# Kernel optimization log

Hardware: AMD Instinct MI355X
Metric: run time of the kernel (lower is better)

## Reference

```python
import jax, jax.numpy as jnp
import numpy as np

D_MODEL = 1024
NUM_HEADS = 16
HEAD_DIM = D_MODEL // NUM_HEADS
BATCH = 2
SEQ = 2048


def setup_inputs() -> dict:
    key = jax.random.key(0)
    ks = jax.random.split(key, 9)
    s = 1.0 / np.sqrt(D_MODEL)
    X = jax.random.normal(ks[0], (BATCH, SEQ, D_MODEL), dtype=jnp.float32)
    # causal mask, broadcastable over batch and heads; masked_fill where mask == 0
    mask = jnp.tril(jnp.ones((SEQ, SEQ), dtype=jnp.int32))[None, None, :, :]
    Wq = jax.random.uniform(ks[1], (D_MODEL, D_MODEL), jnp.float32, -s, s)
    bq = jax.random.uniform(ks[2], (D_MODEL,), jnp.float32, -s, s)
    Wk = jax.random.uniform(ks[3], (D_MODEL, D_MODEL), jnp.float32, -s, s)
    bk = jax.random.uniform(ks[4], (D_MODEL,), jnp.float32, -s, s)
    Wv = jax.random.uniform(ks[5], (D_MODEL, D_MODEL), jnp.float32, -s, s)
    bv = jax.random.uniform(ks[6], (D_MODEL,), jnp.float32, -s, s)
    Wo = jax.random.uniform(ks[7], (D_MODEL, D_MODEL), jnp.float32, -s, s)
    bo = jax.random.uniform(ks[8], (D_MODEL,), jnp.float32, -s, s)
    return {"X": X, "mask": mask, "Wq": Wq, "bq": bq, "Wk": Wk, "bk": bk,
            "Wv": Wv, "bv": bv, "Wo": Wo, "bo": bo}


def reference(X, mask, Wq, bq, Wk, bk, Wv, bv, Wo, bo):
    B, S, _ = X.shape
    scale = 1.0 / np.sqrt(HEAD_DIM).astype(np.float32)

    def split_heads(t):  # [B,S,D] -> [B,H,S,Dh]
        return t.reshape(B, S, NUM_HEADS, HEAD_DIM).transpose(0, 2, 1, 3)

    q = split_heads(X @ Wq.T + bq)
    k = split_heads(X @ Wk.T + bk)
    v = split_heads(X @ Wv.T + bv)
    # [B,H,S,S] attention logits (explicitly materialized, as in the source)
    logits = jnp.einsum("bhqd,bhkd->bhqk", q, k) * scale
    logits = jnp.where(mask == 0, -jnp.inf, logits)
    attn = jax.nn.softmax(logits, axis=-1)  # dropout in eval mode: identity
    ctx = jnp.einsum("bhqk,bhkd->bhqd", attn, v)
    ctx = ctx.transpose(0, 2, 1, 3).reshape(B, S, D_MODEL)
    return ctx @ Wo.T + bo
```

## Files before the change

### kernel.cpp

```cpp
#include <hip/hip_runtime.h>


#define B_   2
#define S_   2048
#define H_   16
#define DH_  64
#define D_   1024
#define M_   (B_ * S_)

typedef __attribute__((ext_vector_type(8))) short short8;
typedef __attribute__((ext_vector_type(4))) short short4_t;
typedef float v4f __attribute__((ext_vector_type(4)));

__device__ __forceinline__ short f2bf(float f) {
    union { float f; unsigned u; } v; v.f = f;
    unsigned r = v.u + 0x7fffu + ((v.u >> 16) & 1u);
    return (short)(r >> 16);
}

#if __has_builtin(__builtin_amdgcn_exp2f)
#define EXP2(x) __builtin_amdgcn_exp2f(x)
#else
#define EXP2(x) exp2f(x)
#endif

__device__ __forceinline__ unsigned pack2(float a, float b) {
    return (__float_as_uint(a) >> 16) | (__float_as_uint(b) & 0xFFFF0000u);
}

__device__ __forceinline__ void gl2lds16(const short* g, short* l) {
    __builtin_amdgcn_global_load_lds(
        (const __attribute__((address_space(1))) unsigned int*)g,
        (__attribute__((address_space(3))) unsigned int*)l,
        16, 0, 0);
}

__global__ __launch_bounds__(256) void cast_kernel(
    const float* __restrict__ X,
    const float* __restrict__ Wq, const float* __restrict__ Wk,
    const float* __restrict__ Wv, const float* __restrict__ Wo,
    short* __restrict__ Xb, short* __restrict__ Wb)
{
    const int NX8 = (M_ * D_) / 8;
    const int NW8 = (D_ * D_) / 8;
    int idx = blockIdx.x * 256 + threadIdx.x;

    const float* src; short* dst; int off;
    if (idx < NX8) { src = X; dst = Xb; off = idx; }
    else {
        int r = idx - NX8;
        int sel = r >> 17;
        int o = r & (NW8 - 1);
        src = (sel == 0) ? Wq : (sel == 1) ? Wk : (sel == 2) ? Wv : Wo;
        dst = Wb + sel * (D_ * D_);
        off = o;
    }
    float4 f0 = ((const float4*)src)[off * 2];
    float4 f1 = ((const float4*)src)[off * 2 + 1];
    short8 s;
    s[0] = f2bf(f0.x); s[1] = f2bf(f0.y); s[2] = f2bf(f0.z); s[3] = f2bf(f0.w);
    s[4] = f2bf(f1.x); s[5] = f2bf(f1.y); s[6] = f2bf(f1.z); s[7] = f2bf(f1.w);
    *(short8*)(dst + (size_t)off * 8) = s;
}

template<int BN, int MODE>
__global__ __launch_bounds__(256) void gemm_kernel(
    const short* __restrict__ A, const short* __restrict__ W,
    const float* __restrict__ bq, const float* __restrict__ bk,
    const float* __restrict__ bv, void* __restrict__ out,
    int M, int N, int K)
{
    constexpr int SM = (MODE == 0) ? 18432 : (8192 + BN * 64);
    __shared__ __align__(16) short smem[SM];
    short* As = smem;
    short* Bs = smem + 8192;

    const int t    = threadIdx.x;
    const int lane = t & 63;
    const int wave = t >> 6;

    const int bid = blockIdx.x;
    const int by  = ((bid & 7) << 2) + ((bid >> 3) & 3);
    const int bx  = bid >> 5;
    const int m0 = by * 128;
    const int n0 = bx * BN;

    const int wm = (wave >> 1) * 64;
    const int wn = (wave & 1) * (BN / 2);
    constexpr int NJ  = BN / 32;
    constexpr int BIT = BN / 32;

    v4f acc[4][NJ] = {};

    const int rsub = lane >> 3;
    const int csw  = ((lane & 7) ^ rsub) * 8;
    const short* Ag = A + (size_t)(m0 + wave * 32 + rsub) * K + csw;
    const short* Wg = W + (size_t)(n0 + wave * (BN / 4) + rsub) * K + csw;
    short* Asw = As + (wave * 32) * 64;
    short* Bsw = Bs + (wave * (BN / 4)) * 64;

    const int lm = lane & 15;
    const int lg = lane >> 4;
    const int lm7 = lm & 7;

    for (int k0 = 0; k0 < K; k0 += 64) {
        #pragma unroll
        for (int i2 = 0; i2 < 4; ++i2)
            gl2lds16(Ag + (size_t)(i2 * 8) * K + k0, Asw + i2 * 512);
        #pragma unroll
        for (int i2 = 0; i2 < BIT; ++i2)
            gl2lds16(Wg + (size_t)(i2 * 8) * K + k0, Bsw + i2 * 512);
        __syncthreads();

        #pragma unroll
        for (int kk = 0; kk < 2; ++kk) {
            const int ch = (kk * 4 + lg) ^ lm7;
            short8 af[4], bf[NJ];
            #pragma unroll
            for (int i = 0; i < 4; ++i)
                af[i] = *(const short8*)((const char*)As + (wm + i * 16 + lm) * 128 + ch * 16);
            #pragma unroll
            for (int j = 0; j < NJ; ++j)
                bf[j] = *(const short8*)((const char*)Bs + (wn + j * 16 + lm) * 128 + ch * 16);
            #pragma unroll
            for (int i = 0; i < 4; ++i)
                #pragma unroll
                for (int j = 0; j < NJ; ++j)
                    acc[i][j] = __builtin_amdgcn_mfma_f32_16x16x32_bf16(af[i], bf[j], acc[i][j], 0, 0, 0);
        }
        __syncthreads();
    }

    const int sel = n0 >> 10;
    const float* bias = (MODE == 2) ? bq : (sel == 0) ? bq : (sel == 1) ? bk : bv;

    if constexpr (MODE == 2) {
        const int colb = n0 + wn + lm;
        const int rowb = m0 + wm + lg * 4;
        #pragma unroll
        for (int j = 0; j < NJ; ++j) {
            int col = colb + j * 16;
            float bv_ = bias[col];
            #pragma unroll
            for (int i = 0; i < 4; ++i)
                #pragma unroll
                for (int r = 0; r < 4; ++r)
                    ((float*)out)[(size_t)(rowb + i * 16 + r) * 1024 + col] = acc[i][j][r] + bv_;
        }
    } else {
        short* Es = smem + wave * (64 * 72);
        const int cb = (n0 + wn) & 1023;
        #pragma unroll
        for (int j = 0; j < 4; ++j) {
            float bv_ = bias[cb + j * 16 + lm];
            #pragma unroll
            for (int i = 0; i < 4; ++i)
                #pragma unroll
                for (int r = 0; r < 4; ++r) {
                    float vv = acc[i][j][r] + bv_;
                    if (sel == 0) vv *= 0.1803368867f;
                    if (sel < 2)
                        Es[(i * 16 + lg * 4 + r) * 72 + j * 16 + lm] = f2bf(vv);
                    else
                        Es[(j * 16 + lm) * 72 + i * 16 + lg * 4 + r] = f2bf(vv);
                }
        }
        __asm__ __volatile__("s_waitcnt lgkmcnt(0)" ::: "memory");
        short* outQKV = (short*)out;
        const int rl = lane >> 3;
        const int c8 = (lane & 7) * 8;
        const int h  = cb >> 6;
        const int b  = (m0 + wm) >> 11;
        const int bh = (b << 4) + h;
        if (sel < 2) {
            #pragma unroll
            for (int it = 0; it < 8; ++it) {
                int row_l = it * 8 + rl;
                short8 vrow = *(const short8*)&Es[row_l * 72 + c8];
                int s = (m0 + wm + row_l) & 2047;
                *(short8*)(outQKV + (size_t)sel * 4194304 +
                           ((size_t)bh * S_ + s) * DH_ + c8) = vrow;
            }
        } else {
            const int s0 = (m0 + wm) & 2047;
            #pragma unroll
            for (int it = 0; it < 8; ++it) {
                int d_l = it * 8 + rl;
                short8 vrow = *(const short8*)&Es[d_l * 72 + c8];
                *(short8*)(outQKV + (size_t)2 * 4194304 +
                           ((size_t)bh << 17) + ((size_t)d_l << 11) + s0 + c8) = vrow;
            }
        }
    }
}

__global__ __launch_bounds__(512, 2) void attn_kernel(
    const short* __restrict__ Q, const short* __restrict__ Kh,
    const short* __restrict__ Vt, short* __restrict__ ctx)
{
    __shared__ __align__(16) short sm[32768];

    const int t    = threadIdx.x;
    const int lane = t & 63;
    const int w    = t >> 6;
    const int wg   = w & 3;
    const int g    = w >> 2;
    const int bid  = blockIdx.x;

    const int lo  = bid & 255;
    const int xcd = lo & 7;
    const int idx = lo >> 3;
    const int bh  = (xcd << 2) + (idx & 3);
    const int jb  = idx >> 2;
    const int j   = (bid < 256) ? jb : (15 - jb);
    const int q0  = j * 128;
    const int nt  = j + 1;
    const int ha  = nt >> 1;
    const int mx  = nt - ha;
    const int pb  = g ? ha : 0;
    const int np  = g ? (nt - ha) : ha;
    const int qr0 = q0 + wg * 32;

    const int lm = lane & 15;
    const int lg = lane >> 4;

    short* Kt = sm + g * 16384;
    short* Vp = Kt + 8192;

    const short* Qb = Q  + (size_t)bh * S_ * DH_;
    const short* Kb = Kh + (size_t)bh * S_ * DH_;
    const short* Vb = Vt + ((size_t)bh << 17);

    const int rsubK = lane >> 3;
    const int cswK  = ((lane & 7) ^ rsubK) * 8;
    const int dV    = wg * 16 + (lane >> 2);
    const int s3V   = dV & 7;

    short8 qf[2][2];
    #pragma unroll
    for (int t2 = 0; t2 < 2; ++t2)
        #pragma unroll
        for (int kk = 0; kk < 2; ++kk)
            qf[t2][kk] = *(const short8*)(Qb + (size_t)(qr0 + t2 * 16 + lm) * DH_ + kk * 32 + lg * 8);

    float m_i[2] = {-1e30f, -1e30f}, l_i[2] = {0.f, 0.f};
    v4f o[2][4] = {};

    for (int tI = 0; tI < mx; ++tI) {
        const bool act   = tI < np;
        const int  kv0   = (pb + tI) * 128;
        const bool dpair = (g == 1) && (tI == mx - 1);

        if (act) {
            #pragma unroll
            for (int i2 = 0; i2 < 4; ++i2) {
                const int rb = wg * 32 + i2 * 8;
                gl2lds16(Kb + (size_t)(kv0 + rb + rsubK) * 64 + cswK, Kt + rb * 64);
            }
            short8 vld[4];
            #pragma unroll
            for (int m = 0; m < 4; ++m) {
                const int cm = (lane & 3) + 4 * m;
                vld[m] = *(const short8*)(Vb + (size_t)dV * 2048 + kv0 + cm * 8);
            }
            char* vrow = (char*)Vp + dV * 256;
            #pragma unroll
            for (int m = 0; m < 4; ++m) {
                const int cm = (lane & 3) + 4 * m;
                const int u  = cm >> 3, kk = (cm >> 2) & 1;
                const int q0off = ((cm & 1) << 4) + ((cm >> 1) & 1) * 4;
                const int bA = (u * 64 + kk * 32 + q0off) * 2;
                const int pA = ((((bA >> 4) ^ s3V) << 4) | (bA & 15));
                const int bB = bA + 16;
                const int pB = ((((bB >> 4) ^ s3V) << 4) | (bB & 15));
                *(short4_t*)(vrow + pA) = __builtin_shufflevector(vld[m], vld[m], 0, 1, 2, 3);
                *(short4_t*)(vrow + pB) = __builtin_shufflevector(vld[m], vld[m], 4, 5, 6, 7);
            }
        }
        __syncthreads();

        if (act) {
            short8 vf[2][2][4];
            #pragma unroll
            for (int u = 0; u < 2; ++u)
                #pragma unroll
                for (int kk = 0; kk < 2; ++kk)
                    #pragma unroll
                    for (int i = 0; i < 4; ++i) {
                        const int d = i * 16 + lm;
                        const int ch = (u * 8 + kk * 4 + lg) ^ (lm & 7);
                        vf[u][kk][i] = *(const short8*)((const char*)Vp + d * 256 + ch * 16);
                    }

            v4f sc[2][2][4] = {};
            #pragma unroll
            for (int u = 0; u < 2; ++u) {
                short8 kf[2][4];
                #pragma unroll
                for (int kk = 0; kk < 2; ++kk)
                    #pragma unroll
                    for (int jj = 0; jj < 4; ++jj) {
                        const int row = u * 64 + jj * 16 + lm;
                        const int ch  = (kk * 4 + lg) ^ (lm & 7);
                        kf[kk][jj] = *(const short8*)((const char*)Kt + row * 128 + ch * 16);
                    }
                #pragma unroll
                for (int kk = 0; kk < 2; ++kk)
                    #pragma unroll
                    for (int t2 = 0; t2 < 2; ++t2)
                        #pragma unroll
                        for (int jj = 0; jj < 4; ++jj)
                            sc[t2][u][jj] = __builtin_amdgcn_mfma_f32_16x16x32_bf16(kf[kk][jj], qf[t2][kk], sc[t2][u][jj], 0, 0, 0);
            }

            float alpha[2];
            short8 pf[2][2][2];
            #pragma unroll
            for (int t2 = 0; t2 < 2; ++t2) {
                float x[2][4][4];
                const int q = qr0 + t2 * 16 + lm;
                #pragma unroll
                for (int u = 0; u < 2; ++u)
                    #pragma unroll
                    for (int jj = 0; jj < 4; ++jj)
                        #pragma unroll
                        for (int r = 0; r < 4; ++r) {
                            float v = sc[t2][u][jj][r];
                            if (dpair && (kv0 + u * 64 + jj * 16 + lg * 4 + r > q)) v = -1e30f;
                            x[u][jj][r] = v;
                        }
                float m8[8];
                #pragma unroll
                for (int z = 0; z < 8; ++z) {
                    const float* xz = x[z >> 2][z & 3];
                    m8[z] = fmaxf(fmaxf(xz[0], xz[1]), fmaxf(xz[2], xz[3]));
                }
                float rm = fmaxf(fmaxf(fmaxf(m8[0], m8[1]), fmaxf(m8[2], m8[3])),
                                 fmaxf(fmaxf(m8[4], m8[5]), fmaxf(m8[6], m8[7])));
                rm = fmaxf(rm, __shfl_xor(rm, 16, 64));
                rm = fmaxf(rm, __shfl_xor(rm, 32, 64));

                const float mn = fmaxf(m_i[t2], rm);
                alpha[t2] = EXP2(m_i[t2] - mn);
                m_i[t2] = mn;

                float s8[8];
                #pragma unroll
                for (int z = 0; z < 8; ++z) {
                    float* xz = x[z >> 2][z & 3];
                    xz[0] = EXP2(xz[0] - mn); xz[1] = EXP2(xz[1] - mn);
                    xz[2] = EXP2(xz[2] - mn); xz[3] = EXP2(xz[3] - mn);
                    s8[z] = (xz[0] + xz[1]) + (xz[2] + xz[3]);
                }
                float rs = ((s8[0] + s8[1]) + (s8[2] + s8[3])) + ((s8[4] + s8[5]) + (s8[6] + s8[7]));
                rs += __shfl_xor(rs, 16, 64);
                rs += __shfl_xor(rs, 32, 64);
                l_i[t2] = l_i[t2] * alpha[t2] + rs;

                #pragma unroll
                for (int u = 0; u < 2; ++u)
                    #pragma unroll
                    for (int kk = 0; kk < 2; ++kk) {
                        union { short8 s; uint4 d; } pk;
                        pk.d.x = pack2(x[u][2 * kk][0],     x[u][2 * kk][1]);
                        pk.d.y = pack2(x[u][2 * kk][2],     x[u][2 * kk][3]);
                        pk.d.z = pack2(x[u][2 * kk + 1][0], x[u][2 * kk + 1][1]);
                        pk.d.w = pack2(x[u][2 * kk + 1][2], x[u][2 * kk + 1][3]);
                        pf[t2][u][kk] = pk.s;
                    }
            }

            #pragma unroll
            for (int t2 = 0; t2 < 2; ++t2)
                #pragma unroll
                for (int i = 0; i < 4; ++i)
                    o[t2][i] *= alpha[t2];

            #pragma unroll
            for (int u = 0; u < 2; ++u)
                #pragma unroll
                for (int kk = 0; kk < 2; ++kk)
                    #pragma unroll
                    for (int t2 = 0; t2 < 2; ++t2)
                        #pragma unroll
                        for (int i = 0; i < 4; ++i)
                            o[t2][i] = __builtin_amdgcn_mfma_f32_16x16x32_bf16(vf[u][kk][i], pf[t2][u][kk], o[t2][i], 0, 0, 0);
        }
        __syncthreads();
    }

    float* fb = (float*)sm;
    if (g == 1) {
        float* mp = &fb[(wg * 64 + lane) * 36];
        mp[0] = m_i[0]; mp[1] = l_i[0]; mp[2] = m_i[1]; mp[3] = l_i[1];
        #pragma unroll
        for (int t2 = 0; t2 < 2; ++t2)
            #pragma unroll
            for (int i = 0; i < 4; ++i)
                #pragma unroll
                for (int r = 0; r < 4; ++r)
                    mp[4 + t2 * 16 + i * 4 + r] = o[t2][i][r];
    }
    __syncthreads();
    if (g == 0) {
        const float* mp = &fb[(wg * 64 + lane) * 36];
        #pragma unroll
        for (int t2 = 0; t2 < 2; ++t2) {
            const float mo = mp[t2 * 2];
            const float lo = mp[t2 * 2 + 1];
            const float mn = fmaxf(m_i[t2], mo);
            const float sa = EXP2(m_i[t2] - mn);
            const float sb = EXP2(mo - mn);
            l_i[t2] = l_i[t2] * sa + lo * sb;
            #pragma unroll
            for (int i = 0; i < 4; ++i)
                #pragma unroll
                for (int r = 0; r < 4; ++r)
                    o[t2][i][r] = o[t2][i][r] * sa + mp[4 + t2 * 16 + i * 4 + r] * sb;
        }

        const int b = bh >> 4, hd = bh & 15;
        #pragma unroll
        for (int t2 = 0; t2 < 2; ++t2) {
            const float inv = 1.f / l_i[t2];
            const size_t base = ((size_t)(b * S_ + qr0 + t2 * 16 + lm) << 10) + (hd << 6) + lg * 4;
            #pragma unroll
            for (int i = 0; i < 4; ++i) {
                short4_t s4;
                #pragma unroll
                for (int r = 0; r < 4; ++r) s4[r] = f2bf(o[t2][i][r] * inv);
                *(short4_t*)(ctx + base + i * 16) = s4;
            }
        }
    }
}

extern "C" void kernel_launch(void* const* d_in, const int* in_sizes, int n_in,
                              void* d_out, int out_size, void* d_ws, size_t ws_size,
                              hipStream_t stream) {
    const float* X  = (const float*)d_in[0];
    const float* Wq = (const float*)d_in[2];
    const float* bq = (const float*)d_in[3];
    const float* Wk = (const float*)d_in[4];
    const float* bk = (const float*)d_in[5];
    const float* Wv = (const float*)d_in[6];
    const float* bv = (const float*)d_in[7];
    const float* Wo = (const float*)d_in[8];
    const float* bo = (const float*)d_in[9];
    float* out = (float*)d_out;

    short* ws  = (short*)d_ws;
    short* Xb  = ws;
    short* Wb  = Xb + 4194304;
    short* Qh  = Wb + 4194304;
    short* Kb  = Qh + 4194304;
    short* Vt  = Kb + 4194304;
    short* Ctx = Vt + 4194304;

    cast_kernel<<<4096, 256, 0, stream>>>(X, Wq, Wk, Wv, Wo, Xb, Wb);

    gemm_kernel<128, 0><<<768, 256, 0, stream>>>(
        Xb, Wb, bq, bk, bv, Qh, M_, 3 * D_, D_);

    attn_kernel<<<512, 512, 0, stream>>>(Qh, Kb, Vt, Ctx);

    gemm_kernel<64, 2><<<512, 256, 0, stream>>>(
        Ctx, Wb + 3145728, bo, bo, bo, out, M_, D_, D_);
}
```

Before: 193.1 us.

## Double-buffer 64-key K/V tiles with prefetch and rebalance split-KV groups

Measured after the change: 188.1 us. -2.6%, faster.

```diff
diff --git a/kernel.cpp b/kernel.cpp
--- a/kernel.cpp
+++ b/kernel.cpp
@@ -214,18 +214,12 @@
     const int jb  = idx >> 2;
     const int j   = (bid < 256) ? jb : (15 - jb);
     const int q0  = j * 128;
-    const int nt  = j + 1;
-    const int ha  = nt >> 1;
-    const int mx  = nt - ha;
-    const int pb  = g ? ha : 0;
-    const int np  = g ? (nt - ha) : ha;
+    const int ng  = j + 1;
+    const int pb  = g * ng;
     const int qr0 = q0 + wg * 32;
 
     const int lm = lane & 15;
     const int lg = lane >> 4;
-
-    short* Kt = sm + g * 16384;
-    short* Vp = Kt + 8192;
 
     const short* Qb = Q  + (size_t)bh * S_ * DH_;
     const short* Kb = Kh + (size_t)bh * S_ * DH_;
@@ -236,6 +230,36 @@
     const int dV    = wg * 16 + (lane >> 2);
     const int s3V   = dV & 7;
 
+    auto stageK = [&](int kv0, short* Kt) {
+        #pragma unroll
+        for (int i2 = 0; i2 < 2; ++i2) {
+            const int rb = wg * 16 + i2 * 8;
+            gl2lds16(Kb + (size_t)(kv0 + rb + rsubK) * 64 + cswK, Kt + rb * 64);
+        }
+    };
+    auto loadV = [&](int kv0, short8* vld) {
+        #pragma unroll
+        for (int m = 0; m < 2; ++m) {
+            const int cm = (lane & 3) + 4 * m;
+            vld[m] = *(const short8*)(Vb + (size_t)dV * 2048 + kv0 + cm * 8);
+        }
+    };
+    auto writeV = [&](const short8* vld, short* Vp) {
+        char* vrow = (char*)Vp + dV * 128;
+        #pragma unroll
+        for (int m = 0; m < 2; ++m) {
+            const int cm = (lane & 3) + 4 * m;
+            const int kk = (cm >> 2) & 1;
+            const int q0off = ((cm & 1) << 4) + ((cm >> 1) & 1) * 4;
+            const int bA = (kk * 32 + q0off) * 2;
+            const int pA = ((((bA >> 4) ^ s3V) << 4) | (bA & 15));
+            const int bB = bA + 16;
+            const int pB = ((((bB >> 4) ^ s3V) << 4) | (bB & 15));
+            *(short4_t*)(vrow + pA) = __builtin_shufflevector(vld[m], vld[m], 0, 1, 2, 3);
+            *(short4_t*)(vrow + pB) = __builtin_shufflevector(vld[m], vld[m], 4, 5, 6, 7);
+        }
+    };
+
     short8 qf[2][2];
     #pragma unroll
     for (int t2 = 0; t2 < 2; ++t2)
@@ -246,147 +270,119 @@
     float m_i[2] = {-1e30f, -1e30f}, l_i[2] = {0.f, 0.f};
     v4f o[2][4] = {};
 
-    for (int tI = 0; tI < mx; ++tI) {
-        const bool act   = tI < np;
-        const int  kv0   = (pb + tI) * 128;
-        const bool dpair = (g == 1) && (tI == mx - 1);
-
-        if (act) {
-            #pragma unroll
-            for (int i2 = 0; i2 < 4; ++i2) {
-                const int rb = wg * 32 + i2 * 8;
-                gl2lds16(Kb + (size_t)(kv0 + rb + rsubK) * 64 + cswK, Kt + rb * 64);
-            }
-            short8 vld[4];
-            #pragma unroll
-            for (int m = 0; m < 4; ++m) {
-                const int cm = (lane & 3) + 4 * m;
-                vld[m] = *(const short8*)(Vb + (size_t)dV * 2048 + kv0 + cm * 8);
-            }
-            char* vrow = (char*)Vp + dV * 256;
-            #pragma unroll
-            for (int m = 0; m < 4; ++m) {
-                const int cm = (lane & 3) + 4 * m;
-                const int u  = cm >> 3, kk = (cm >> 2) & 1;
-                const int q0off = ((cm & 1) << 4) + ((cm >> 1) & 1) * 4;
-                const int bA = (u * 64 + kk * 32 + q0off) * 2;
-                const int pA = ((((bA >> 4) ^ s3V) << 4) | (bA & 15));
-                const int bB = bA + 16;
-                const int pB = ((((bB >> 4) ^ s3V) << 4) | (bB & 15));
-                *(short4_t*)(vrow + pA) = __builtin_shufflevector(vld[m], vld[m], 0, 1, 2, 3);
-                *(short4_t*)(vrow + pB) = __builtin_shufflevector(vld[m], vld[m], 4, 5, 6, 7);
-            }
-        }
+    short8 vpre[2];
+    short* gB = sm + g * 16384;
+    stageK(pb * 64, gB);
+    loadV(pb * 64, vpre);
+    writeV(vpre, gB + 4096);
+    __syncthreads();
+
+    int cur = 0;
+    for (int it = 0; it < ng; ++it) {
+        const int kv0 = (pb + it) * 64;
+        const bool pre = (it + 1 < ng);
+        short* Kt = gB + cur * 8192;
+        short* Vp = Kt + 4096;
+        const bool dmask = (kv0 + 63) > qr0;
+
+        if (pre) {
+            stageK(kv0 + 64, gB + (cur ^ 1) * 8192);
+            loadV(kv0 + 64, vpre);
+        }
+
+        short8 vf[2][4];
+        #pragma unroll
+        for (int kk = 0; kk < 2; ++kk)
+            #pragma unroll
+            for (int i = 0; i < 4; ++i) {
+                const int d = i * 16 + lm;
+                const int ch = (kk * 4 + lg) ^ (lm & 7);
+                vf[kk][i] = *(const short8*)((const char*)Vp + d * 128 + ch * 16);
+            }
+
+        short8 kf[2][4];
+        #pragma unroll
+        for (int kk = 0; kk < 2; ++kk)
+            #pragma unroll
+            for (int jj = 0; jj < 4; ++jj) {
+                const int row = jj * 16 + lm;
+                const int ch  = (kk * 4 + lg) ^ (lm & 7);
+                kf[kk][jj] = *(const short8*)((const char*)Kt + row * 128 + ch * 16);
+            }
+        v4f sc[2][4] = {};
+        #pragma unroll
+        for (int kk = 0; kk < 2; ++kk)
+            #pragma unroll
+            for (int t2 = 0; t2 < 2; ++t2)
+                #pragma unroll
+                for (int jj = 0; jj < 4; ++jj)
+                    sc[t2][jj] = __builtin_amdgcn_mfma_f32_16x16x32_bf16(kf[kk][jj], qf[t2][kk], sc[t2][jj], 0, 0, 0);
+
+        float alpha[2];
+        short8 pf[2][2];
+        #pragma unroll
+        for (int t2 = 0; t2 < 2; ++t2) {
+            float x[4][4];
+            const int q = qr0 + t2 * 16 + lm;
+            #pragma unroll
+            for (int jj = 0; jj < 4; ++jj)
+                #pragma unroll
+                for (int r = 0; r < 4; ++r) {
+                    float v = sc[t2][jj][r];
+                    if (dmask && (kv0 + jj * 16 + lg * 4 + r > q)) v = -1e30f;
+                    x[jj][r] = v;
+                }
+            float m4[4];
+            #pragma unroll
+            for (int jj = 0; jj < 4; ++jj)
+                m4[jj] = fmaxf(fmaxf(x[jj][0], x[jj][1]), fmaxf(x[jj][2], x[jj][3]));
+            float rm = fmaxf(fmaxf(m4[0], m4[1]), fmaxf(m4[2], m4[3]));
+            rm = fmaxf(rm, __shfl_xor(rm, 16, 64));
+            rm = fmaxf(rm, __shfl_xor(rm, 32, 64));
+
+            const float mn = fmaxf(m_i[t2], rm);
+            alpha[t2] = EXP2(m_i[t2] - mn);
+            m_i[t2] = mn;
+            float s4[4];
+            #pragma unroll
+            for (int jj = 0; jj < 4; ++jj) {
+                x[jj][0] = EXP2(x[jj][0] - mn); x[jj][1] = EXP2(x[jj][1] - mn);
+                x[jj][2] = EXP2(x[jj][2] - mn); x[jj][3] = EXP2(x[jj][3] - mn);
+                s4[jj] = (x[jj][0] + x[jj][1]) + (x[jj][2] + x[jj][3]);
+            }
+            float rs = (s4[0] + s4[1]) + (s4[2] + s4[3]);
+            rs += __shfl_xor(rs, 16, 64);
+            rs += __shfl_xor(rs, 32, 64);
+            l_i[t2] = l_i[t2] * alpha[t2] + rs;
+
+            #pragma unroll
+            for (int kk = 0; kk < 2; ++kk) {
+                union { short8 s; uint4 d; } pk;
+                pk.d.x = pack2(x[2 * kk][0],     x[2 * kk][1]);
+                pk.d.y = pack2(x[2 * kk][2],     x[2 * kk][3]);
+                pk.d.z = pack2(x[2 * kk + 1][0], x[2 * kk + 1][1]);
+                pk.d.w = pack2(x[2 * kk + 1][2], x[2 * kk + 1][3]);
+                pf[t2][kk] = pk.s;
+            }
+        }
+
+        #pragma unroll
+        for (int t2 = 0; t2 < 2; ++t2)
+            #pragma unroll
+            for (int i = 0; i < 4; ++i)
+                o[t2][i] *= alpha[t2];
+
+        #pragma unroll
+        for (int kk = 0; kk < 2; ++kk)
+            #pragma unroll
+            for (int t2 = 0; t2 < 2; ++t2)
+                #pragma unroll
+                for (int i = 0; i < 4; ++i)
+                    o[t2][i] = __builtin_amdgcn_mfma_f32_16x16x32_bf16(vf[kk][i], pf[t2][kk], o[t2][i], 0, 0, 0);
+
+        if (pre) writeV(vpre, gB + (cur ^ 1) * 8192 + 4096);
         __syncthreads();
-
-        if (act) {
-            short8 vf[2][2][4];
-            #pragma unroll
-            for (int u = 0; u < 2; ++u)
-                #pragma unroll
-                for (int kk = 0; kk < 2; ++kk)
-                    #pragma unroll
-                    for (int i = 0; i < 4; ++i) {
-                        const int d = i * 16 + lm;
-                        const int ch = (u * 8 + kk * 4 + lg) ^ (lm & 7);
-                        vf[u][kk][i] = *(const short8*)((const char*)Vp + d * 256 + ch * 16);
-                    }
-
-            v4f sc[2][2][4] = {};
-            #pragma unroll
-            for (int u = 0; u < 2; ++u) {
-                short8 kf[2][4];
-                #pragma unroll
-                for (int kk = 0; kk < 2; ++kk)
-                    #pragma unroll
-                    for (int jj = 0; jj < 4; ++jj) {
-                        const int row = u * 64 + jj * 16 + lm;
-                        const int ch  = (kk * 4 + lg) ^ (lm & 7);
-                        kf[kk][jj] = *(const short8*)((const char*)Kt + row * 128 + ch * 16);
-                    }
-                #pragma unroll
-                for (int kk = 0; kk < 2; ++kk)
-                    #pragma unroll
-                    for (int t2 = 0; t2 < 2; ++t2)
-                        #pragma unroll
-                        for (int jj = 0; jj < 4; ++jj)
-                            sc[t2][u][jj] = __builtin_amdgcn_mfma_f32_16x16x32_bf16(kf[kk][jj], qf[t2][kk], sc[t2][u][jj], 0, 0, 0);
-            }
-
-            float alpha[2];
-            short8 pf[2][2][2];
-            #pragma unroll
-            for (int t2 = 0; t2 < 2; ++t2) {
-                float x[2][4][4];
-                const int q = qr0 + t2 * 16 + lm;
-                #pragma unroll
-                for (int u = 0; u < 2; ++u)
-                    #pragma unroll
-                    for (int jj = 0; jj < 4; ++jj)
-                        #pragma unroll
-                        for (int r = 0; r < 4; ++r) {
-                            float v = sc[t2][u][jj][r];
-                            if (dpair && (kv0 + u * 64 + jj * 16 + lg * 4 + r > q)) v = -1e30f;
-                            x[u][jj][r] = v;
-                        }
-                float m8[8];
-                #pragma unroll
-                for (int z = 0; z < 8; ++z) {
-                    const float* xz = x[z >> 2][z & 3];
-                    m8[z] = fmaxf(fmaxf(xz[0], xz[1]), fmaxf(xz[2], xz[3]));
-                }
-                float rm = fmaxf(fmaxf(fmaxf(m8[0], m8[1]), fmaxf(m8[2], m8[3])),
-                                 fmaxf(fmaxf(m8[4], m8[5]), fmaxf(m8[6], m8[7])));
-                rm = fmaxf(rm, __shfl_xor(rm, 16, 64));
-                rm = fmaxf(rm, __shfl_xor(rm, 32, 64));
-
-                const float mn = fmaxf(m_i[t2], rm);
-                alpha[t2] = EXP2(m_i[t2] - mn);
-                m_i[t2] = mn;
-
-                float s8[8];
-                #pragma unroll
-                for (int z = 0; z < 8; ++z) {
-                    float* xz = x[z >> 2][z & 3];
-                    xz[0] = EXP2(xz[0] - mn); xz[1] = EXP2(xz[1] - mn);
-                    xz[2] = EXP2(xz[2] - mn); xz[3] = EXP2(xz[3] - mn);
-                    s8[z] = (xz[0] + xz[1]) + (xz[2] + xz[3]);
-                }
-                float rs = ((s8[0] + s8[1]) + (s8[2] + s8[3])) + ((s8[4] + s8[5]) + (s8[6] + s8[7]));
-                rs += __shfl_xor(rs, 16, 64);
-                rs += __shfl_xor(rs, 32, 64);
-                l_i[t2] = l_i[t2] * alpha[t2] + rs;
-
-                #pragma unroll
-                for (int u = 0; u < 2; ++u)
-                    #pragma unroll
-                    for (int kk = 0; kk < 2; ++kk) {
-                        union { short8 s; uint4 d; } pk;
-                        pk.d.x = pack2(x[u][2 * kk][0],     x[u][2 * kk][1]);
-                        pk.d.y = pack2(x[u][2 * kk][2],     x[u][2 * kk][3]);
-                        pk.d.z = pack2(x[u][2 * kk + 1][0], x[u][2 * kk + 1][1]);
-                        pk.d.w = pack2(x[u][2 * kk + 1][2], x[u][2 * kk + 1][3]);
-                        pf[t2][u][kk] = pk.s;
-                    }
-            }
-
-            #pragma unroll
-            for (int t2 = 0; t2 < 2; ++t2)
-                #pragma unroll
-                for (int i = 0; i < 4; ++i)
-                    o[t2][i] *= alpha[t2];
-
-            #pragma unroll
-            for (int u = 0; u < 2; ++u)
-                #pragma unroll
-                for (int kk = 0; kk < 2; ++kk)
-                    #pragma unroll
-                    for (int t2 = 0; t2 < 2; ++t2)
-                        #pragma unroll
-                        for (int i = 0; i < 4; ++i)
-                            o[t2][i] = __builtin_amdgcn_mfma_f32_16x16x32_bf16(vf[u][kk][i], pf[t2][u][kk], o[t2][i], 0, 0, 0);
-        }
-        __syncthreads();
+        cur ^= 1;
     }
 
     float* fb = (float*)sm;
```
